# Kernel tuning notes

Measured on AMD Instinct MI355X. Metric: run time of the kernel, lower is better.

## Reference

```python
import jax, jax.numpy as jnp
import numpy as np

HEADS = 4
OUT_F = 32
EDGE_F = 16
ALPHA = 0.2  # LeakyReLU negative slope


def setup_inputs() -> dict:
    key = jax.random.key(0)
    k1, k2, k3, k4, k5 = jax.random.split(key, 5)
    N, E, IN_F = 20000, 640000, 128
    h = jax.random.normal(k1, (N, IN_F), dtype=jnp.float32)
    edge_index = jax.random.randint(k2, (2, E), 0, N, dtype=jnp.int64)
    edge_attr = jax.random.normal(k3, (E, EDGE_F), dtype=jnp.float32)
    # xavier_uniform-like scale for params
    W = jax.random.normal(k4, (IN_F, HEADS * OUT_F), dtype=jnp.float32) * 0.1
    a = jax.random.normal(k5, (HEADS, 2 * OUT_F + EDGE_F), dtype=jnp.float32) * 0.1
    return {"h": h, "edge_index": edge_index, "edge_attr": edge_attr, "W": W, "a": a}


def reference(h, edge_index, edge_attr, W, a):
    N = h.shape[0]
    # Wh: [N, heads, out]
    Wh = (h @ W).reshape(N, HEADS, OUT_F)
    src = edge_index[0]
    dst = edge_index[1]
    # Split attention vector a = [a_src | a_dst | a_edge] to avoid materializing
    # the [E, heads, 2*out+edge_f] concat tensor (same math as einsum on concat).
    a_src = a[:, :OUT_F]            # [h, out]
    a_dst = a[:, OUT_F:2 * OUT_F]   # [h, out]
    a_edge = a[:, 2 * OUT_F:]       # [h, edge_f]
    e = (jnp.einsum('ehd,hd->eh', Wh[src], a_src)
         + jnp.einsum('ehd,hd->eh', Wh[dst], a_dst)
         + edge_attr @ a_edge.T)    # [E, heads]
    e = jnp.where(e >= 0, e, ALPHA * e)  # LeakyReLU
    # NOTE: original applies softmax over the HEADS dim (dim=1), per edge.
    attention = jax.nn.softmax(e, axis=1)  # [E, heads]
    # dropout p=0.0 (eval): identity
    msg = attention[:, :, None] * Wh[dst]  # [E, heads, out]
    h_prime = jnp.zeros_like(Wh).at[src].add(msg)  # scatter-add over src nodes
    out = h_prime.reshape(N, HEADS * OUT_F)
    return jax.nn.elu(out)
```

## Files before the change

kernel.cpp:

```cpp
#include <hip/hip_runtime.h>
#include <math.h>

#define HEADS 4
#define OUT_F 32
#define EDGE_F 16
#define ALPHA 0.2f
#define CF 128
#define IN_F 128
#define AROW (2*OUT_F+EDGE_F)
#define BCOLS 144
#define IMG_USHORTS (BCOLS * IN_F)
#define MAXDEG 80

typedef __attribute__((ext_vector_type(4))) unsigned short us4;
typedef __attribute__((ext_vector_type(8))) short s16x8;
typedef __attribute__((ext_vector_type(4))) float f32x4;

static __device__ __forceinline__ unsigned short f2b(float x) {
    union { float f; unsigned u; } v; v.f = x;
    unsigned r = v.u + 0x7FFFu + ((v.u >> 16) & 1u);
    return (unsigned short)(r >> 16);
}
static __device__ __forceinline__ float b2f(unsigned short u) {
    union { unsigned u32; float f; } v; v.u32 = ((unsigned)u) << 16;
    return v.f;
}

static __device__ __forceinline__ int img_idx(int c, int k) {
    int cb = c >> 4, cl = c & 15;
    int ks = k >> 5, q = (k >> 3) & 3, j = k & 7;
    return (((cb * 4 + ks) * 64) + q * 16 + cl) * 8 + j;
}

__global__ __launch_bounds__(256) void k_init(const float* __restrict__ W,
                                              const float* __restrict__ a,
                                              unsigned short* __restrict__ WtImg,
                                              int* __restrict__ cursor, int N)
{
    int tid = threadIdx.x;
    int b = blockIdx.x;

    if (b < 8) {
        __shared__ float aSD[8][32];
        {
            int g = tid >> 5, c = tid & 31;
            aSD[g][c] = a[(g & 3) * AROW + ((g & 4) ? OUT_F : 0) + c];
        }
        __syncthreads();

        for (int i = b * 256 + tid; i < IN_F * CF; i += 8 * 256) {
            int k = i >> 7, c = i & 127;
            WtImg[img_idx(c, k)] = f2b(W[i]);
        }
        if (b == 0 && tid < IN_F) {
            const float* wr = W + (size_t)tid * CF;
            #pragma unroll
            for (int j = 0; j < 8; ++j) {
                const float* av = aSD[j];
                const float* wc = wr + (j & 3) * OUT_F;
                float s = 0.f;
                #pragma unroll 8
                for (int c = 0; c < 32; ++c) s = fmaf(wc[c], av[c], s);
                WtImg[img_idx(128 + j, tid)] = f2b(s);
            }
            #pragma unroll
            for (int cc = 136; cc < BCOLS; ++cc)
                WtImg[img_idx(cc, tid)] = 0;
        }
    } else {
        int i = (b - 8) * 256 + tid;
        if (i < N) cursor[i] = 0;
    }
}

__global__ __launch_bounds__(256) void k_gemm_fill(const float* __restrict__ h,
                                                   const unsigned short* __restrict__ WtImg,
                                                   const float* __restrict__ ea,
                                                   const float* __restrict__ a,
                                                   const int* __restrict__ ei,
                                                   unsigned short* __restrict__ Whb,
                                                   float* __restrict__ ssrc,
                                                   float* __restrict__ sdst,
                                                   int* __restrict__ cursor,
                                                   int4* __restrict__ recs,
                                                   int N, int E, int GB)
{
    __shared__ float ae[64];
    int tid = threadIdx.x;
    int b = blockIdx.x;

    if (b < GB) {
        int l = tid & 63, wv = tid >> 6;
        int q = l >> 4, c_ = l & 15;
        int rbase = b * 64 + wv * 16;

        int arow = rbase + c_;
        if (arow >= N) arow = N - 1;
        const float* hp_ = h + (size_t)arow * IN_F + q * 8;
        s16x8 afr[4];
        #pragma unroll
        for (int ks = 0; ks < 4; ++ks) {
            float4 x = *(const float4*)(hp_ + ks * 32);
            float4 y = *(const float4*)(hp_ + ks * 32 + 4);
            s16x8 f;
            f[0] = (short)f2b(x.x); f[1] = (short)f2b(x.y);
            f[2] = (short)f2b(x.z); f[3] = (short)f2b(x.w);
            f[4] = (short)f2b(y.x); f[5] = (short)f2b(y.y);
            f[6] = (short)f2b(y.z); f[7] = (short)f2b(y.w);
            afr[ks] = f;
        }

        const s16x8* bimg = (const s16x8*)WtImg;
        f32x4 acc[9];
        #pragma unroll
        for (int cb = 0; cb < 9; ++cb) acc[cb] = (f32x4){0.f, 0.f, 0.f, 0.f};
        #pragma unroll
        for (int cb = 0; cb < 9; ++cb) {
            #pragma unroll
            for (int ks = 0; ks < 4; ++ks) {
                s16x8 bfr = bimg[(cb * 4 + ks) * 64 + l];
                acc[cb] = __builtin_amdgcn_mfma_f32_16x16x32_bf16(afr[ks], bfr, acc[cb], 0, 0, 0);
            }
        }

        #pragma unroll
        for (int reg = 0; reg < 4; ++reg) {
            int row = rbase + q * 4 + reg;
            if (row < N) {
                size_t ro = (size_t)row * CF + c_;
                #pragma unroll
                for (int cb = 0; cb < 8; ++cb)
                    Whb[ro + cb * 16] = f2b(acc[cb][reg]);
            }
        }
        if (c_ < 8) {
            #pragma unroll
            for (int reg = 0; reg < 4; ++reg) {
                int row = rbase + q * 4 + reg;
                if (row < N) {
                    float v = acc[8][reg];
                    if (c_ < 4) ssrc[row * HEADS + c_] = v;
                    else        sdst[row * HEADS + (c_ - 4)] = v;
                }
            }
        }
    } else {
        if (tid < 64) ae[tid] = a[(tid >> 4) * AROW + 2 * OUT_F + (tid & 15)];
        __syncthreads();

        int e0 = (b - GB) * 512 + tid * 2;
        if (e0 >= E) return;
        int n = (E - e0 < 2) ? (E - e0) : 2;

        int s[2], d[2];
        if (n == 2) {
            int2 s2 = *(const int2*)(ei + e0);
            int2 d2 = *(const int2*)(ei + E + e0);
            s[0] = s2.x; s[1] = s2.y;
            d[0] = d2.x; d[1] = d2.y;
        } else {
            s[0] = ei[e0]; d[0] = ei[E + e0];
            s[1] = 0;      d[1] = 0;
        }

        #pragma unroll
        for (int k = 0; k < 2; ++k) {
            if (k >= n) break;
            int e = e0 + k;
            const float* eav = ea + (size_t)e * EDGE_F;
            float4 v0 = *(const float4*)(eav + 0);
            float4 v1 = *(const float4*)(eav + 4);
            float4 v2 = *(const float4*)(eav + 8);
            float4 v3 = *(const float4*)(eav + 12);
            float dv[HEADS];
            #pragma unroll
            for (int g = 0; g < HEADS; ++g) {
                const float* av = ae + g * EDGE_F;
                dv[g] = v0.x*av[0] + v0.y*av[1] + v0.z*av[2] + v0.w*av[3]
                      + v1.x*av[4] + v1.y*av[5] + v1.z*av[6] + v1.w*av[7]
                      + v2.x*av[8] + v2.y*av[9] + v2.z*av[10] + v2.w*av[11]
                      + v3.x*av[12] + v3.y*av[13] + v3.z*av[14] + v3.w*av[15];
            }
            unsigned lo = (unsigned)f2b(dv[0]) | ((unsigned)f2b(dv[1]) << 16);
            unsigned hi = (unsigned)f2b(dv[2]) | ((unsigned)f2b(dv[3]) << 16);
            int rk = atomicAdd(&cursor[s[k]], 1);
            if (rk < MAXDEG)
                recs[(size_t)s[k] * MAXDEG + rk] = make_int4(d[k], (int)lo, (int)hi, 0);
        }
    }
}

__global__ __launch_bounds__(256) void k_aggregate(const int* __restrict__ cursor,
                                                   const int4* __restrict__ recs,
                                                   const float* __restrict__ ssrc,
                                                   const float* __restrict__ sdst,
                                                   const unsigned short* __restrict__ Whb,
                                                   float* __restrict__ out,
                                                   int N)
{
    int wave = threadIdx.x >> 6;
    int lane = threadIdx.x & 63;
    int node = blockIdx.x * 4 + wave;
    if (node >= N) return;

    int deg = cursor[node];
    if (deg > MAXDEG) deg = MAXDEG;
    int beg = node * MAXDEG;
    int end = beg + deg;
    int l = lane & 31;
    int half = lane >> 5;
    int c0 = l * 4;
    int hh = l >> 3;

    float ssh = ssrc[(size_t)node * HEADS + hh];

    float ac0 = 0.f, ac1 = 0.f, ac2 = 0.f, ac3 = 0.f;
    for (int i2 = beg; i2 < end; i2 += 8) {
        #pragma unroll
        for (int u = 0; u < 4; ++u) {
            int idx = i2 + u * 2 + half;
            bool live = (idx < end);
            int4 r = live ? recs[idx] : make_int4(0, 0, 0, 0);
            int di = r.x;
            float sdh = sdst[(size_t)di * HEADS + hh];
            unsigned w32 = (hh & 2) ? (unsigned)r.z : (unsigned)r.y;
            unsigned short eh = (hh & 1) ? (unsigned short)(w32 >> 16)
                                         : (unsigned short)(w32 & 0xFFFFu);
            float e = ssh + sdh + b2f(eh);
            e = (e >= 0.f) ? e : ALPHA * e;
            float p = __expf(e);
            float sum = p + __shfl_xor(p, 8);
            sum += __shfl_xor(sum, 16);
            float at = live ? p / sum : 0.f;

            us4 w = *(const us4*)(Whb + (size_t)di * CF + c0);
            ac0 = fmaf(at, b2f(w.x), ac0);
            ac1 = fmaf(at, b2f(w.y), ac1);
            ac2 = fmaf(at, b2f(w.z), ac2);
            ac3 = fmaf(at, b2f(w.w), ac3);
        }
    }
    ac0 += __shfl_xor(ac0, 32);
    ac1 += __shfl_xor(ac1, 32);
    ac2 += __shfl_xor(ac2, 32);
    ac3 += __shfl_xor(ac3, 32);

    if (half == 0) {
        ac0 = (ac0 > 0.f) ? ac0 : (__expf(ac0) - 1.f);
        ac1 = (ac1 > 0.f) ? ac1 : (__expf(ac1) - 1.f);
        ac2 = (ac2 > 0.f) ? ac2 : (__expf(ac2) - 1.f);
        ac3 = (ac3 > 0.f) ? ac3 : (__expf(ac3) - 1.f);
        *(float4*)(out + (size_t)node * CF + c0) = make_float4(ac0, ac1, ac2, ac3);
    }
}

extern "C" void kernel_launch(void* const* d_in, const int* in_sizes, int n_in,
                              void* d_out, int out_size, void* d_ws, size_t ws_size,
                              hipStream_t stream)
{
    const float* h  = (const float*)d_in[0];
    const int*   ei = (const int*)d_in[1];
    const float* ea = (const float*)d_in[2];
    const float* W  = (const float*)d_in[3];
    const float* a  = (const float*)d_in[4];
    float* out = (float*)d_out;

    int N = in_sizes[0] / IN_F;
    int E = in_sizes[1] / 2;

    char* ws = (char*)d_ws;
    int4*           recs   = (int4*)ws;           ws += (size_t)N * MAXDEG * sizeof(int4);
    unsigned short* Whb    = (unsigned short*)ws; ws += (size_t)N * CF * sizeof(unsigned short);
    unsigned short* WtImg  = (unsigned short*)ws; ws += (size_t)IMG_USHORTS * sizeof(unsigned short);
    float*          ssrc   = (float*)ws;          ws += (size_t)N * HEADS * sizeof(float);
    float*          sdst   = (float*)ws;          ws += (size_t)N * HEADS * sizeof(float);
    int*            cursor = (int*)ws;            ws += (size_t)N * sizeof(int);

    k_init<<<8 + (N + 255) / 256, 256, 0, stream>>>(W, a, WtImg, cursor, N);

    int GB = (N + 63) / 64;
    int EB = (E + 511) / 512;
    k_gemm_fill<<<GB + EB, 256, 0, stream>>>(h, WtImg, ea, a, ei, Whb, ssrc, sdst,
                                             cursor, recs, N, E, GB);

    k_aggregate<<<(N + 3) / 4, 256, 0, stream>>>(cursor, recs, ssrc, sdst,
                                                 Whb, out, N);
}
```

Before: 102.3 us.

## Precompute per-edge softmax in fill kernel and pack quantized weights into 64-bit records

Splits the fused GEMM+fill kernel into separate GEMM and fill kernels so the fill stage can read ssrc/sdst and compute the full per-edge head softmax up front. Attention weights are quantized to 12 bits each and packed with a 16-bit destination index into a u64 record, halving record size. The aggregation kernel broadcasts records via shuffles and only does the gather-FMA. This drops the sdst gathers and exp work from aggregation, in exchange for losing the overlap of GEMM with fill, 12-bit attention precision, and a limit of 65536 on node indices.

```diff
diff --git a/kernel.cpp b/kernel.cpp
--- a/kernel.cpp
+++ b/kernel.cpp
@@ -15,6 +15,7 @@
 typedef __attribute__((ext_vector_type(4))) unsigned short us4;
 typedef __attribute__((ext_vector_type(8))) short s16x8;
 typedef __attribute__((ext_vector_type(4))) float f32x4;
+typedef unsigned long long u64;
 
 static __device__ __forceinline__ unsigned short f2b(float x) {
     union { float f; unsigned u; } v; v.f = x;
@@ -73,130 +74,131 @@
     }
 }
 
-__global__ __launch_bounds__(256) void k_gemm_fill(const float* __restrict__ h,
-                                                   const unsigned short* __restrict__ WtImg,
-                                                   const float* __restrict__ ea,
-                                                   const float* __restrict__ a,
-                                                   const int* __restrict__ ei,
-                                                   unsigned short* __restrict__ Whb,
-                                                   float* __restrict__ ssrc,
-                                                   float* __restrict__ sdst,
-                                                   int* __restrict__ cursor,
-                                                   int4* __restrict__ recs,
-                                                   int N, int E, int GB)
-{
-    __shared__ float ae[64];
+__global__ __launch_bounds__(256) void k_gemm(const float* __restrict__ h,
+                                              const unsigned short* __restrict__ WtImg,
+                                              unsigned short* __restrict__ Whb,
+                                              float* __restrict__ ssrc,
+                                              float* __restrict__ sdst,
+                                              int N)
+{
     int tid = threadIdx.x;
     int b = blockIdx.x;
 
-    if (b < GB) {
-        int l = tid & 63, wv = tid >> 6;
-        int q = l >> 4, c_ = l & 15;
-        int rbase = b * 64 + wv * 16;
-
-        int arow = rbase + c_;
-        if (arow >= N) arow = N - 1;
-        const float* hp_ = h + (size_t)arow * IN_F + q * 8;
-        s16x8 afr[4];
+    int l = tid & 63, wv = tid >> 6;
+    int q = l >> 4, c_ = l & 15;
+    int rbase = b * 64 + wv * 16;
+
+    int arow = rbase + c_;
+    if (arow >= N) arow = N - 1;
+    const float* hp_ = h + (size_t)arow * IN_F + q * 8;
+    s16x8 afr[4];
+    #pragma unroll
+    for (int ks = 0; ks < 4; ++ks) {
+        float4 x = *(const float4*)(hp_ + ks * 32);
+        float4 y = *(const float4*)(hp_ + ks * 32 + 4);
+        s16x8 f;
+        f[0] = (short)f2b(x.x); f[1] = (short)f2b(x.y);
+        f[2] = (short)f2b(x.z); f[3] = (short)f2b(x.w);
+        f[4] = (short)f2b(y.x); f[5] = (short)f2b(y.y);
+        f[6] = (short)f2b(y.z); f[7] = (short)f2b(y.w);
+        afr[ks] = f;
+    }
+
+    const s16x8* bimg = (const s16x8*)WtImg;
+    f32x4 acc[9];
+    #pragma unroll
+    for (int cb = 0; cb < 9; ++cb) acc[cb] = (f32x4){0.f, 0.f, 0.f, 0.f};
+    #pragma unroll
+    for (int cb = 0; cb < 9; ++cb) {
         #pragma unroll
         for (int ks = 0; ks < 4; ++ks) {
-            float4 x = *(const float4*)(hp_ + ks * 32);
-            float4 y = *(const float4*)(hp_ + ks * 32 + 4);
-            s16x8 f;
-            f[0] = (short)f2b(x.x); f[1] = (short)f2b(x.y);
-            f[2] = (short)f2b(x.z); f[3] = (short)f2b(x.w);
-            f[4] = (short)f2b(y.x); f[5] = (short)f2b(y.y);
-            f[6] = (short)f2b(y.z); f[7] = (short)f2b(y.w);
-            afr[ks] = f;
-        }
-
-        const s16x8* bimg = (const s16x8*)WtImg;
-        f32x4 acc[9];
-        #pragma unroll
-        for (int cb = 0; cb < 9; ++cb) acc[cb] = (f32x4){0.f, 0.f, 0.f, 0.f};
-        #pragma unroll
-        for (int cb = 0; cb < 9; ++cb) {
-            #pragma unroll
-            for (int ks = 0; ks < 4; ++ks) {
-                s16x8 bfr = bimg[(cb * 4 + ks) * 64 + l];
-                acc[cb] = __builtin_amdgcn_mfma_f32_16x16x32_bf16(afr[ks], bfr, acc[cb], 0, 0, 0);
-            }
-        }
-
+            s16x8 bfr = bimg[(cb * 4 + ks) * 64 + l];
+            acc[cb] = __builtin_amdgcn_mfma_f32_16x16x32_bf16(afr[ks], bfr, acc[cb], 0, 0, 0);
+        }
+    }
+
+    #pragma unroll
+    for (int reg = 0; reg < 4; ++reg) {
+        int row = rbase + q * 4 + reg;
+        if (row < N) {
+            size_t ro = (size_t)row * CF + c_;
+            #pragma unroll
+            for (int cb = 0; cb < 8; ++cb)
+                Whb[ro + cb * 16] = f2b(acc[cb][reg]);
+        }
+    }
+    if (c_ < 8) {
         #pragma unroll
         for (int reg = 0; reg < 4; ++reg) {
             int row = rbase + q * 4 + reg;
             if (row < N) {
-                size_t ro = (size_t)row * CF + c_;
-                #pragma unroll
-                for (int cb = 0; cb < 8; ++cb)
-                    Whb[ro + cb * 16] = f2b(acc[cb][reg]);
+                float v = acc[8][reg];
+                if (c_ < 4) ssrc[row * HEADS + c_] = v;
+                else        sdst[row * HEADS + (c_ - 4)] = v;
             }
         }
-        if (c_ < 8) {
-            #pragma unroll
-            for (int reg = 0; reg < 4; ++reg) {
-                int row = rbase + q * 4 + reg;
-                if (row < N) {
-                    float v = acc[8][reg];
-                    if (c_ < 4) ssrc[row * HEADS + c_] = v;
-                    else        sdst[row * HEADS + (c_ - 4)] = v;
-                }
-            }
-        }
-    } else {
-        if (tid < 64) ae[tid] = a[(tid >> 4) * AROW + 2 * OUT_F + (tid & 15)];
-        __syncthreads();
-
-        int e0 = (b - GB) * 512 + tid * 2;
-        if (e0 >= E) return;
-        int n = (E - e0 < 2) ? (E - e0) : 2;
-
-        int s[2], d[2];
-        if (n == 2) {
-            int2 s2 = *(const int2*)(ei + e0);
-            int2 d2 = *(const int2*)(ei + E + e0);
-            s[0] = s2.x; s[1] = s2.y;
-            d[0] = d2.x; d[1] = d2.y;
-        } else {
-            s[0] = ei[e0]; d[0] = ei[E + e0];
-            s[1] = 0;      d[1] = 0;
-        }
-
-        #pragma unroll
-        for (int k = 0; k < 2; ++k) {
-            if (k >= n) break;
-            int e = e0 + k;
-            const float* eav = ea + (size_t)e * EDGE_F;
-            float4 v0 = *(const float4*)(eav + 0);
-            float4 v1 = *(const float4*)(eav + 4);
-            float4 v2 = *(const float4*)(eav + 8);
-            float4 v3 = *(const float4*)(eav + 12);
-            float dv[HEADS];
-            #pragma unroll
-            for (int g = 0; g < HEADS; ++g) {
-                const float* av = ae + g * EDGE_F;
-                dv[g] = v0.x*av[0] + v0.y*av[1] + v0.z*av[2] + v0.w*av[3]
-                      + v1.x*av[4] + v1.y*av[5] + v1.z*av[6] + v1.w*av[7]
-                      + v2.x*av[8] + v2.y*av[9] + v2.z*av[10] + v2.w*av[11]
-                      + v3.x*av[12] + v3.y*av[13] + v3.z*av[14] + v3.w*av[15];
-            }
-            unsigned lo = (unsigned)f2b(dv[0]) | ((unsigned)f2b(dv[1]) << 16);
-            unsigned hi = (unsigned)f2b(dv[2]) | ((unsigned)f2b(dv[3]) << 16);
-            int rk = atomicAdd(&cursor[s[k]], 1);
-            if (rk < MAXDEG)
-                recs[(size_t)s[k] * MAXDEG + rk] = make_int4(d[k], (int)lo, (int)hi, 0);
-        }
-    }
-}
-
-__global__ __launch_bounds__(256) void k_aggregate(const int* __restrict__ cursor,
-                                                   const int4* __restrict__ recs,
-                                                   const float* __restrict__ ssrc,
-                                                   const float* __restrict__ sdst,
-                                                   const unsigned short* __restrict__ Whb,
-                                                   float* __restrict__ out,
-                                                   int N)
+    }
+}
+
+__global__ __launch_bounds__(256) void k_fill(const int* __restrict__ ei,
+                                              const float* __restrict__ ea,
+                                              const float* __restrict__ a,
+                                              const float* __restrict__ ssrc,
+                                              const float* __restrict__ sdst,
+                                              int* __restrict__ cursor,
+                                              u64* __restrict__ recs,
+                                              int E)
+{
+    __shared__ float ae[64];
+    int tid = threadIdx.x;
+    if (tid < 64) ae[tid] = a[(tid >> 4) * AROW + 2 * OUT_F + (tid & 15)];
+    __syncthreads();
+
+    int e = blockIdx.x * 256 + tid;
+    if (e >= E) return;
+
+    int s = ei[e];
+    int d = ei[E + e];
+    float4 sa = *(const float4*)(ssrc + (size_t)s * HEADS);
+    float4 sd = *(const float4*)(sdst + (size_t)d * HEADS);
+    const float* eav = ea + (size_t)e * EDGE_F;
+    float4 v0 = *(const float4*)(eav + 0);
+    float4 v1 = *(const float4*)(eav + 4);
+    float4 v2 = *(const float4*)(eav + 8);
+    float4 v3 = *(const float4*)(eav + 12);
+
+    float ev[HEADS];
+    float base[HEADS] = { sa.x + sd.x, sa.y + sd.y, sa.z + sd.z, sa.w + sd.w };
+    #pragma unroll
+    for (int g = 0; g < HEADS; ++g) {
+        const float* av = ae + g * EDGE_F;
+        float dotv = v0.x*av[0] + v0.y*av[1] + v0.z*av[2] + v0.w*av[3]
+                   + v1.x*av[4] + v1.y*av[5] + v1.z*av[6] + v1.w*av[7]
+                   + v2.x*av[8] + v2.y*av[9] + v2.z*av[10] + v2.w*av[11]
+                   + v3.x*av[12] + v3.y*av[13] + v3.z*av[14] + v3.w*av[15];
+        float x = base[g] + dotv;
+        ev[g] = (x >= 0.f) ? x : ALPHA * x;
+    }
+    float m = fmaxf(fmaxf(ev[0], ev[1]), fmaxf(ev[2], ev[3]));
+    float p0 = __expf(ev[0] - m), p1 = __expf(ev[1] - m);
+    float p2 = __expf(ev[2] - m), p3 = __expf(ev[3] - m);
+    float inv = 4095.f / (p0 + p1 + p2 + p3);
+    unsigned q0 = (unsigned)(p0 * inv + 0.5f);
+    unsigned q1 = (unsigned)(p1 * inv + 0.5f);
+    unsigned q2 = (unsigned)(p2 * inv + 0.5f);
+    unsigned q3 = (unsigned)(p3 * inv + 0.5f);
+    u64 rec = (u64)(unsigned)d | ((u64)q0 << 16) | ((u64)q1 << 28)
+            | ((u64)q2 << 40) | ((u64)q3 << 52);
+
+    int rk = atomicAdd(&cursor[s], 1);
+    if (rk < MAXDEG) recs[(size_t)s * MAXDEG + rk] = rec;
+}
+
+__global__ __launch_bounds__(256) void k_agg(const int* __restrict__ cursor,
+                                             const u64* __restrict__ recs,
+                                             const unsigned short* __restrict__ Whb,
+                                             float* __restrict__ out,
+                                             int N)
 {
     int wave = threadIdx.x >> 6;
     int lane = threadIdx.x & 63;
@@ -205,53 +207,39 @@
 
     int deg = cursor[node];
     if (deg > MAXDEG) deg = MAXDEG;
-    int beg = node * MAXDEG;
-    int end = beg + deg;
-    int l = lane & 31;
-    int half = lane >> 5;
-    int c0 = l * 4;
-    int hh = l >> 3;
-
-    float ssh = ssrc[(size_t)node * HEADS + hh];
-
-    float ac0 = 0.f, ac1 = 0.f, ac2 = 0.f, ac3 = 0.f;
-    for (int i2 = beg; i2 < end; i2 += 8) {
-        #pragma unroll
-        for (int u = 0; u < 4; ++u) {
-            int idx = i2 + u * 2 + half;
-            bool live = (idx < end);
-            int4 r = live ? recs[idx] : make_int4(0, 0, 0, 0);
-            int di = r.x;
-            float sdh = sdst[(size_t)di * HEADS + hh];
-            unsigned w32 = (hh & 2) ? (unsigned)r.z : (unsigned)r.y;
-            unsigned short eh = (hh & 1) ? (unsigned short)(w32 >> 16)
-                                         : (unsigned short)(w32 & 0xFFFFu);
-            float e = ssh + sdh + b2f(eh);
-            e = (e >= 0.f) ? e : ALPHA * e;
-            float p = __expf(e);
-            float sum = p + __shfl_xor(p, 8);
-            sum += __shfl_xor(sum, 16);
-            float at = live ? p / sum : 0.f;
-
-            us4 w = *(const us4*)(Whb + (size_t)di * CF + c0);
-            ac0 = fmaf(at, b2f(w.x), ac0);
-            ac1 = fmaf(at, b2f(w.y), ac1);
-            ac2 = fmaf(at, b2f(w.z), ac2);
-            ac3 = fmaf(at, b2f(w.w), ac3);
-        }
-    }
-    ac0 += __shfl_xor(ac0, 32);
-    ac1 += __shfl_xor(ac1, 32);
-    ac2 += __shfl_xor(ac2, 32);
-    ac3 += __shfl_xor(ac3, 32);
-
-    if (half == 0) {
-        ac0 = (ac0 > 0.f) ? ac0 : (__expf(ac0) - 1.f);
-        ac1 = (ac1 > 0.f) ? ac1 : (__expf(ac1) - 1.f);
-        ac2 = (ac2 > 0.f) ? ac2 : (__expf(ac2) - 1.f);
-        ac3 = (ac3 > 0.f) ? ac3 : (__expf(ac3) - 1.f);
-        *(float4*)(out + (size_t)node * CF + c0) = make_float4(ac0, ac1, ac2, ac3);
-    }
+    int base = node * MAXDEG;
+    int c0 = lane * 2;
+    int hh = lane >> 4;
+    int sh = 16 + 12 * hh;
+
+    float ac0 = 0.f, ac1 = 0.f;
+
+    for (int c = 0; c < deg; c += 64) {
+        int m = deg - c;
+        if (m > 64) m = 64;
+        int2 r_own = make_int2(0, 0);
+        if (lane < m) r_own = ((const int2*)recs)[base + c + lane];
+
+        for (int i = 0; i < m; i += 4) {
+            #pragma unroll
+            for (int u = 0; u < 4; ++u) {
+                int idx = i + u;
+                if (idx >= m) break;
+                int rx = __shfl(r_own.x, idx);
+                int ry = __shfl(r_own.y, idx);
+                u64 r = ((u64)(unsigned)ry << 32) | (unsigned)rx;
+                int di = rx & 0xFFFF;
+                float at = (float)((unsigned)((r >> sh) & 0xFFFu)) * (1.f / 4095.f);
+                ushort2 w = *(const ushort2*)(Whb + (size_t)di * CF + c0);
+                ac0 = fmaf(at, b2f(w.x), ac0);
+                ac1 = fmaf(at, b2f(w.y), ac1);
+            }
+        }
+    }
+
+    ac0 = (ac0 > 0.f) ? ac0 : (__expf(ac0) - 1.f);
+    ac1 = (ac1 > 0.f) ? ac1 : (__expf(ac1) - 1.f);
+    *(float2*)(out + (size_t)node * CF + c0) = make_float2(ac0, ac1);
 }
 
 extern "C" void kernel_launch(void* const* d_in, const int* in_sizes, int n_in,
@@ -269,7 +257,7 @@
     int E = in_sizes[1] / 2;
 
     char* ws = (char*)d_ws;
-    int4*           recs   = (int4*)ws;           ws += (size_t)N * MAXDEG * sizeof(int4);
+    u64*            recs   = (u64*)ws;            ws += (size_t)N * MAXDEG * sizeof(u64);
     unsigned short* Whb    = (unsigned short*)ws; ws += (size_t)N * CF * sizeof(unsigned short);
     unsigned short* WtImg  = (unsigned short*)ws; ws += (size_t)IMG_USHORTS * sizeof(unsigned short);
     float*          ssrc   = (float*)ws;          ws += (size_t)N * HEADS * sizeof(float);
@@ -279,10 +267,10 @@
     k_init<<<8 + (N + 255) / 256, 256, 0, stream>>>(W, a, WtImg, cursor, N);
 
     int GB = (N + 63) / 64;
-    int EB = (E + 511) / 512;
-    k_gemm_fill<<<GB + EB, 256, 0, stream>>>(h, WtImg, ea, a, ei, Whb, ssrc, sdst,
-                                             cursor, recs, N, E, GB);
-
-    k_aggregate<<<(N + 3) / 4, 256, 0, stream>>>(cursor, recs, ssrc, sdst,
-                                                 Whb, out, N);
-}
+    k_gemm<<<GB, 256, 0, stream>>>(h, WtImg, Whb, ssrc, sdst, N);
+
+    k_fill<<<(E + 255) / 256, 256, 0, stream>>>(ei, ea, a, ssrc, sdst,
+                                                cursor, recs, E);
+
+    k_agg<<<(N + 3) / 4, 256, 0, stream>>>(cursor, recs, Whb, out, N);
+}
```

After: 108.2 us. +5.8%, slower.
